# Kernel optimization log

Measured on AMD Instinct MI355X. Metric: run time of the kernel, lower is better.

The kernel has to match this reference:

```python
import jax, jax.numpy as jnp
import numpy as np

B, C, CO, N = 2, 32, 32, 64
MODES, LMAX, RBINS = 16, 2, 16
HALF = MODES // 2
NL = (LMAX + 1) ** 2  # 9 real spherical harmonics up to l=2
M = MODES ** 3
HID = 16  # round(CO * 0.5)


def _build_basis():
    # frequencies of the kept FNO corner modes along each axis
    f = np.concatenate([np.arange(HALF), np.arange(-HALF, 0)]).astype(np.float32)
    kx, ky, kz = np.meshgrid(f, f, f, indexing='ij')
    kx, ky, kz = kx.ravel(), ky.ravel(), kz.ravel()
    r = np.sqrt(kx ** 2 + ky ** 2 + kz ** 2)
    nzm = (r > 0).astype(np.float32)
    inv = np.where(r > 0, 1.0 / np.maximum(r, 1e-9), 0.0)
    ux, uy, uz = kx * inv, ky * inv, kz * inv
    # real spherical harmonics l=0,1,2 (cartesian form); all l>0 vanish at DC
    Y = np.stack([
        0.282095 * np.ones_like(r),
        0.488603 * uy, 0.488603 * uz, 0.488603 * ux,
        1.092548 * ux * uy, 1.092548 * uy * uz,
        0.315392 * (3.0 * uz ** 2 - nzm),
        1.092548 * ux * uz, 0.546274 * (ux ** 2 - uy ** 2)], axis=0)  # [NL, M]
    shell = np.minimum((r / (r.max() + 1e-6) * RBINS).astype(np.int64), RBINS - 1)
    cnt = np.bincount(shell, minlength=RBINS).astype(np.float32)
    w = 1.0 / np.sqrt(np.maximum(cnt, 1.0))
    mask = (shell[None, :] == np.arange(RBINS)[:, None]).astype(np.float32) * w[:, None]  # [RBINS, M]
    return (mask[:, None, :] * Y[None]).reshape(RBINS * NL, M).astype(np.float32)

BASIS = jnp.asarray(_build_basis())  # [K=144, M=4096], fixed projection basis
IDX = jnp.asarray(np.concatenate([np.arange(HALF), np.arange(N - HALF, N)]))  # kept mode indices


def cgelu(z):
    return jax.nn.gelu(z.real) + 1j * jax.nn.gelu(z.imag)


def setup_inputs() -> dict:
    key = jax.random.key(0)
    ks = jax.random.split(key, 17)
    rn = lambda k, s: jax.random.normal(k, s, dtype=jnp.float32)
    return {
        'x': rn(ks[0], (B, C, N, N, N)),
        'w_fno_r': rn(ks[1], (CO, C)) * 0.1, 'w_fno_i': rn(ks[2], (CO, C)) * 0.1,
        'b_fno_r': rn(ks[3], (CO,)) * 0.1, 'b_fno_i': rn(ks[4], (CO,)) * 0.1,
        'w_gate_r': rn(ks[5], (CO,)), 'w_gate_i': rn(ks[6], (CO,)),
        'w_spec_r': rn(ks[7], (RBINS, NL, C, CO)) * 0.1, 'w_spec_i': rn(ks[8], (RBINS, NL, C, CO)) * 0.1,
        'mlp_w1_r': rn(ks[9], (HID, CO)) * 0.1, 'mlp_w1_i': rn(ks[10], (HID, CO)) * 0.1,
        'mlp_b1_r': rn(ks[11], (HID,)) * 0.1, 'mlp_b1_i': rn(ks[12], (HID,)) * 0.1,
        'mlp_w2_r': rn(ks[13], (CO, HID)) * 0.1, 'mlp_w2_i': rn(ks[14], (CO, HID)) * 0.1,
        'mlp_b2_r': rn(ks[15], (CO,)) * 0.1, 'mlp_b2_i': rn(ks[16], (CO,)) * 0.1,
    }


def reference(x, w_fno_r, w_fno_i, b_fno_r, b_fno_i, w_gate_r, w_gate_i,
              w_spec_r, w_spec_i, mlp_w1_r, mlp_w1_i, mlp_b1_r, mlp_b1_i,
              mlp_w2_r, mlp_w2_i, mlp_b2_r, mlp_b2_i):
    cx = lambda r, i: (r + 1j * i).astype(jnp.complex64)
    xc = x.astype(jnp.complex64)
    w_fno, b_fno = cx(w_fno_r, w_fno_i), cx(b_fno_r, b_fno_i)
    w_gate = cx(w_gate_r, w_gate_i)
    w_spec = cx(w_spec_r, w_spec_i)
    w1, b1 = cx(mlp_w1_r, mlp_w1_i), cx(mlp_b1_r, mlp_b1_i)
    w2, b2 = cx(mlp_w2_r, mlp_w2_i), cx(mlp_b2_r, mlp_b2_i)

    # skip paths: complex 1x1-conv ('linear') and complex soft-gating
    skip_fno = jnp.einsum('oc,bcxyz->boxyz', w_fno, xc) + b_fno[None, :, None, None, None]
    skip_mlp = xc * w_gate[None, :, None, None, None]

    # Harmonic layer: FFT -> slice kept modes -> harmonic/radial projection
    # -> complex spectral conv -> inverse projection -> scatter -> iFFT
    xf = jnp.fft.fftn(xc, axes=(-3, -2, -1))
    xs = xf[:, :, IDX[:, None, None], IDX[None, :, None], IDX[None, None, :]].reshape(B, C, M)
    coeffs = jnp.einsum('bcm,km->bck', xs, BASIS).reshape(B, C, RBINS, NL)
    coeffs = jnp.einsum('bisl,slio->bosl', coeffs, w_spec)
    xs2 = jnp.einsum('bck,km->bcm', coeffs.reshape(B, CO, RBINS * NL), BASIS)
    full = jnp.zeros((B, CO, N, N, N), jnp.complex64).at[
        :, :, IDX[:, None, None], IDX[None, :, None], IDX[None, None, :]
    ].set(xs2.reshape(B, CO, MODES, MODES, MODES))
    x_fno = jnp.fft.ifftn(full, axes=(-3, -2, -1))

    x1 = x_fno + skip_fno  # n_layers=1 -> no activation here
    h = cgelu(jnp.einsum('hc,bcxyz->bhxyz', w1, x1) + b1[None, :, None, None, None])
    y = jnp.einsum('oh,bhxyz->boxyz', w2, h) + b2[None, :, None, None, None]
    return (y + skip_mlp).real
```

## Files before the change

### kernel.cpp

```cpp
#include <hip/hip_runtime.h>
#include <hip/hip_bf16.h>

#define PI2 6.283185307179586f

typedef __attribute__((ext_vector_type(8))) short short8;
typedef __attribute__((ext_vector_type(4))) float f32x4;

static const size_t O_Y      = 0;
static const size_t O_W1RT   = 36864;
static const size_t O_W1IT   = 37376;
static const size_t O_W1XR   = 37888;
static const size_t O_W1XI   = 38400;
static const size_t O_B1PR   = 38912;
static const size_t O_B1PI   = 38928;
static const size_t O_WSH    = 38944;
static const size_t O_SHELL  = 38960;
static const size_t O_ORDER  = 43056;
static const size_t O_SSTART = 47152;
static const size_t O_COEF   = 47232;
static const size_t O_COEF2  = 65664;
static const size_t O_XS     = 84096;
static const size_t O_XS2    = 608384;
static const size_t O_T2     = 1132672;
static const size_t O_T1     = 3229824;

static __device__ __forceinline__ float geluf(float v) {
  float u = 0.7978845608028654f * (v + 0.044715f * v * v * v);
  float a = fabsf(u);
  float e = __expf(-2.0f * a);
  float th = (1.0f - e) / (1.0f + e);
  th = copysignf(th, u);
  return 0.5f * v * (1.0f + th);
}

static __device__ __forceinline__ unsigned int f2bfbits(float f) {
  unsigned int u = __float_as_uint(f);
  u += 0x7fffu + ((u >> 16) & 1u);
  return u >> 16;
}

static __device__ __forceinline__ unsigned int pk2(float a, float b) {
  return f2bfbits(a) | (f2bfbits(b) << 16);
}

__global__ __launch_bounds__(256) void k0_init(
    const float* __restrict__ wfr, const float* __restrict__ wfi,
    const float* __restrict__ bfr, const float* __restrict__ bfi,
    const float* __restrict__ w1r, const float* __restrict__ w1i,
    const float* __restrict__ b1r, const float* __restrict__ b1i,
    float* __restrict__ ws) {
  float* Y    = ws + O_Y;
  float* w1rt = ws + O_W1RT;  float* w1it = ws + O_W1IT;
  float* W1xr = ws + O_W1XR;  float* W1xi = ws + O_W1XI;
  float* b1pr = ws + O_B1PR;  float* b1pi = ws + O_B1PI;
  float* wsh  = ws + O_WSH;
  int* shellOf = (int*)(ws + O_SHELL);
  int* order   = (int*)(ws + O_ORDER);
  int* sstart  = (int*)(ws + O_SSTART);

  __shared__ int cnt[16], fill[16], st[17];
  int tid = threadIdx.x;
  if (tid < 16) { cnt[tid] = 0; fill[tid] = 0; }
  __syncthreads();
  for (int m = tid; m < 4096; m += 256) {
    int ix = m >> 8, iy = (m >> 4) & 15, iz = m & 15;
    float kx = (float)(ix < 8 ? ix : ix - 16);
    float ky = (float)(iy < 8 ? iy : iy - 16);
    float kz = (float)(iz < 8 ? iz : iz - 16);
    float r2 = kx*kx + ky*ky + kz*kz;
    float r  = sqrtf(r2);
    float nzm = r2 > 0.f ? 1.f : 0.f;
    float inv = r2 > 0.f ? 1.0f / fmaxf(r, 1e-9f) : 0.f;
    float ux = kx*inv, uy = ky*inv, uz = kz*inv;
    Y[0*4096+m] = 0.282095f;
    Y[1*4096+m] = 0.488603f * uy;
    Y[2*4096+m] = 0.488603f * uz;
    Y[3*4096+m] = 0.488603f * ux;
    Y[4*4096+m] = 1.092548f * ux*uy;
    Y[5*4096+m] = 1.092548f * uy*uz;
    Y[6*4096+m] = 0.315392f * (3.0f*uz*uz - nzm);
    Y[7*4096+m] = 1.092548f * ux*uz;
    Y[8*4096+m] = 0.546274f * (ux*ux - uy*uy);
    float rmax = sqrtf(192.0f);
    float t = r / (rmax + 1e-6f) * 16.0f;
    int sh = (int)t; sh = sh > 15 ? 15 : sh;
    shellOf[m] = sh;
    atomicAdd(&cnt[sh], 1);
  }
  __syncthreads();
  if (tid == 0) { int a = 0; for (int s = 0; s < 16; ++s) { st[s] = a; a += cnt[s]; } st[16] = a; }
  __syncthreads();
  if (tid < 16) wsh[tid] = 1.0f / sqrtf(fmaxf((float)cnt[tid], 1.0f));
  if (tid < 17) sstart[tid] = st[tid];
  for (int m = tid; m < 4096; m += 256) {
    int sh = shellOf[m];
    int p = atomicAdd(&fill[sh], 1);
    order[st[sh] + p] = m;
  }
  for (int e = tid; e < 512; e += 256) {
    int j = e >> 5, c = e & 31;
    float ar = 0.f, ai = 0.f;
    for (int o = 0; o < 32; ++o) {
      float wr_ = w1r[j*32+o], wi_ = w1i[j*32+o];
      float fr  = wfr[o*32+c], fi_ = wfi[o*32+c];
      ar += wr_*fr - wi_*fi_;
      ai += wr_*fi_ + wi_*fr;
    }
    W1xr[c*16+j] = ar;  W1xi[c*16+j] = ai;
    w1rt[c*16+j] = w1r[j*32+c];
    w1it[c*16+j] = w1i[j*32+c];
  }
  if (tid < 16) {
    int j = tid;
    float ar = b1r[j], ai = b1i[j];
    for (int o = 0; o < 32; ++o) {
      ar += w1r[j*32+o]*bfr[o] - w1i[j*32+o]*bfi[o];
      ai += w1r[j*32+o]*bfi[o] + w1i[j*32+o]*bfr[o];
    }
    b1pr[j] = ar; b1pi[j] = ai;
  }
}

__global__ __launch_bounds__(256) void k12_fwd(const float* __restrict__ x, float* __restrict__ T2) {
  __shared__ __align__(16) float zS[4096];
  __shared__ float2 slab[64*17];
  __shared__ float2 tw[16*17];
  float* zP = zS;  float* zQ = zS + 1024;  float* zB = zS + 2048;  float* zD = zS + 3072;
  float* ysum = zS;
  int blk = blockIdx.x;
  const float* src = x + (size_t)blk * 4096;
  int tid = threadIdx.x;

  {
    int y = tid >> 2, zt = tid & 3;
    const float4* s4 = (const float4*)(src + y*64);
    float4 u0 = s4[zt];
    float4 u1 = s4[zt + 4];
    float4 u2 = s4[zt + 8];
    float4 u3 = s4[zt + 12];
    const float* p0 = (const float*)&u0; const float* p1 = (const float*)&u1;
    const float* p2 = (const float*)&u2; const float* p3 = (const float*)&u3;
    int base = 4*zt*64 + y;
    #pragma unroll
    for (int e = 0; e < 4; ++e) {
      float a = p0[e] + p2[e], c = p1[e] + p3[e];
      float bb = p0[e] - p2[e], d = p1[e] - p3[e];
      zP[base + e*64] = a + c;
      zQ[base + e*64] = a - c;
      zB[base + e*64] = bb;
      zD[base + e*64] = d;
    }
  }
  {
    int k = tid >> 4, i2 = tid & 15;
    float f = (float)(k < 8 ? k : k - 16);
    float ang = -PI2 * f * (float)i2 / 64.0f;
    float sw, cw; __sincosf(ang, &sw, &cw);
    tw[k*17 + i2] = make_float2(cw, sw);
  }
  __syncthreads();

  {
    int kz = tid & 15, yq = tid >> 4;
    int j = kz & 3;
    const float2* twp = tw + kz*17;
    float arr[4] = {0.f,0.f,0.f,0.f}, aii[4] = {0.f,0.f,0.f,0.f};
    if ((j & 1) == 0) {
      const float* plane = (j == 0) ? zP : zQ;
      #pragma unroll
      for (int z0 = 0; z0 < 16; ++z0) {
        float2 w = twp[z0];
        float4 s = *(const float4*)&plane[z0*64 + 4*yq];
        arr[0] += s.x*w.x; aii[0] += s.x*w.y;
        arr[1] += s.y*w.x; aii[1] += s.y*w.y;
        arr[2] += s.z*w.x; aii[2] += s.z*w.y;
        arr[3] += s.w*w.x; aii[3] += s.w*w.y;
      }
    } else {
      float dsg = (j == 1) ? -1.f : 1.f;
      #pragma unroll
      for (int z0 = 0; z0 < 16; ++z0) {
        float2 w = twp[z0];
        float4 b = *(const float4*)&zB[z0*64 + 4*yq];
        float4 d = *(const float4*)&zD[z0*64 + 4*yq];
        float swi = dsg * w.y, swr = dsg * w.x;
        arr[0] += b.x*w.x - d.x*swi;  aii[0] += b.x*w.y + d.x*swr;
        arr[1] += b.y*w.x - d.y*swi;  aii[1] += b.y*w.y + d.y*swr;
        arr[2] += b.z*w.x - d.z*swi;  aii[2] += b.z*w.y + d.z*swr;
        arr[3] += b.w*w.x - d.w*swi;  aii[3] += b.w*w.y + d.w*swr;
      }
    }
    int y0 = 4*yq;
    slab[(y0+0)*17 + kz] = make_float2(arr[0], aii[0]);
    slab[(y0+1)*17 + kz] = make_float2(arr[1], aii[1]);
    slab[(y0+2)*17 + kz] = make_float2(arr[2], aii[2]);
    slab[(y0+3)*17 + kz] = make_float2(arr[3], aii[3]);
  }
  __syncthreads();

  {
    int y0 = tid >> 4, kz = tid & 15;
    float2 u0 = slab[(y0     )*17 + kz];
    float2 u1 = slab[(y0 + 16)*17 + kz];
    float2 u2 = slab[(y0 + 32)*17 + kz];
    float2 u3 = slab[(y0 + 48)*17 + kz];
    float Ar = u0.x + u2.x, Ai = u0.y + u2.y;
    float Br = u0.x - u2.x, Bi = u0.y - u2.y;
    float Cr = u1.x + u3.x, Ci = u1.y + u3.y;
    float Dr = u1.x - u3.x, Di = u1.y - u3.y;
    float* yp = ysum + y0*162 + kz*10;
    yp[0] = Ar + Cr;  yp[1] = Ai + Ci;
    yp[2] = Br + Di;  yp[3] = Bi - Dr;
    yp[4] = Ar - Cr;  yp[5] = Ai - Ci;
    yp[6] = Br - Di;  yp[7] = Bi + Dr;
  }
  __syncthreads();

  {
    int kz = tid & 15, kyi = tid >> 4;
    const float* yp = ysum + kz*10 + (kyi & 3)*2;
    const float2* twp = tw + kyi*17;
    float ar = 0.f, ai = 0.f;
    #pragma unroll
    for (int y0 = 0; y0 < 16; ++y0) {
      float sr = yp[y0*162], si = yp[y0*162 + 1];
      float2 w = twp[y0];
      ar += sr*w.x - si*w.y;
      ai += sr*w.y + si*w.x;
    }
    *(float2*)&T2[(size_t)blk*512 + (kyi*16 + kz)*2] = make_float2(ar, ai);
  }
}

__global__ __launch_bounds__(256) void k3_dftx(const float* __restrict__ T2, float* __restrict__ xs) {
  __shared__ float slab[64*34];
  __shared__ float xsum[2592];
  __shared__ float2 twx[16*17];
  int blk = blockIdx.x;
  int bc = blk >> 4, ky = blk & 15;
  int tid = threadIdx.x;
  for (int i = tid; i < 2048; i += 256) {
    int xr = i >> 5, rem = i & 31;
    slab[xr*34 + rem] = T2[((size_t)(bc*64 + xr)*16 + ky)*32 + rem];
  }
  {
    int k = tid >> 4, i2 = tid & 15;
    float f = (float)(k < 8 ? k : k - 16);
    float ang = -PI2 * f * (float)i2 / 64.0f;
    float sw, cw; __sincosf(ang, &sw, &cw);
    twx[k*17 + i2] = make_float2(cw, sw);
  }
  __syncthreads();
  {
    int x0 = tid >> 4, kz = tid & 15;
    const float2* sp = (const float2*)slab;
    float2 u0 = sp[(x0     )*17 + kz];
    float2 u1 = sp[(x0 + 16)*17 + kz];
    float2 u2 = sp[(x0 + 32)*17 + kz];
    float2 u3 = sp[(x0 + 48)*17 + kz];
    float Ar = u0.x + u2.x, Ai = u0.y + u2.y;
    float Br = u0.x - u2.x, Bi = u0.y - u2.y;
    float Cr = u1.x + u3.x, Ci = u1.y + u3.y;
    float Dr = u1.x - u3.x, Di = u1.y - u3.y;
    float* yp = xsum + x0*162 + kz*10;
    yp[0] = Ar + Cr;  yp[1] = Ai + Ci;
    yp[2] = Br + Di;  yp[3] = Bi - Dr;
    yp[4] = Ar - Cr;  yp[5] = Ai - Ci;
    yp[6] = Br - Di;  yp[7] = Bi + Dr;
  }
  __syncthreads();
  {
    int kz = tid & 15, kxi = tid >> 4;
    const float* yp = xsum + kz*10 + (kxi & 3)*2;
    const float2* twp = twx + kxi*17;
    float ar = 0.f, ai = 0.f;
    #pragma unroll
    for (int x0 = 0; x0 < 16; ++x0) {
      float sr = yp[x0*162], si = yp[x0*162 + 1];
      float2 w = twp[x0];
      ar += sr*w.x - si*w.y;
      ai += sr*w.y + si*w.x;
    }
    *(float2*)&xs[(size_t)bc*8192 + (kxi*256 + ky*16 + kz)*2] = make_float2(ar, ai);
  }
}

__global__ __launch_bounds__(256) void k4_proj(const float* __restrict__ xs, const float* __restrict__ Y,
    const int* __restrict__ order, const int* __restrict__ sstart, const float* __restrict__ wsh,
    float* __restrict__ coeffs) {
  int blk = blockIdx.x; int bc = blk >> 4, s = blk & 15;
  int tid = threadIdx.x;
  int st = sstart[s], en = sstart[s+1];
  float ar[9], ai[9];
  #pragma unroll
  for (int l = 0; l < 9; ++l) { ar[l] = 0.f; ai[l] = 0.f; }
  for (int ii = st + tid; ii < en; ii += 256) {
    int m = order[ii];
    float2 v = *(const float2*)&xs[(size_t)bc*8192 + m*2];
    #pragma unroll
    for (int l = 0; l < 9; ++l) {
      float yv = Y[l*4096 + m];
      ar[l] += yv * v.x; ai[l] += yv * v.y;
    }
  }
  __shared__ float red[256*19];
  #pragma unroll
  for (int l = 0; l < 9; ++l) { red[tid*19 + l] = ar[l]; red[tid*19 + 9 + l] = ai[l]; }
  __syncthreads();
  for (int r = 128; r >= 1; r >>= 1) {
    if (tid < r) {
      #pragma unroll
      for (int q = 0; q < 18; ++q) red[tid*19 + q] += red[(tid + r)*19 + q];
    }
    __syncthreads();
  }
  if (tid == 0) {
    float w = wsh[s];
    for (int l = 0; l < 9; ++l) {
      coeffs[((size_t)bc*144 + s*9 + l)*2]     = w * red[l];
      coeffs[((size_t)bc*144 + s*9 + l)*2 + 1] = w * red[9 + l];
    }
  }
}

__global__ __launch_bounds__(64) void k5_spec(const float* __restrict__ coeffs,
    const float* __restrict__ wsr, const float* __restrict__ wsi, float* __restrict__ coeffs2) {
  int blk = blockIdx.x;
  int b = blk / 144, sl = blk % 144;
  int o = threadIdx.x;
  if (o >= 32) return;
  float ar = 0.f, ai = 0.f;
  for (int i = 0; i < 32; ++i) {
    float cr = coeffs[((size_t)(b*32 + i)*144 + sl)*2];
    float ci = coeffs[((size_t)(b*32 + i)*144 + sl)*2 + 1];
    float wr = wsr[(sl*32 + i)*32 + o];
    float wi = wsi[(sl*32 + i)*32 + o];
    ar += cr*wr - ci*wi;
    ai += cr*wi + ci*wr;
  }
  const float sc = 1.0f / 262144.0f;
  coeffs2[((size_t)(b*32 + o)*144 + sl)*2]     = ar * sc;
  coeffs2[((size_t)(b*32 + o)*144 + sl)*2 + 1] = ai * sc;
}

__global__ __launch_bounds__(256) void k7_unproj(const float* __restrict__ coeffs2, const float* __restrict__ Y,
    const int* __restrict__ shellOf, const float* __restrict__ wsh, float* __restrict__ xs2) {
  int bo = blockIdx.x >> 4;
  int m = ((blockIdx.x & 15) << 8) | threadIdx.x;
  __shared__ float c2[288];
  for (int i = threadIdx.x; i < 288; i += 256) c2[i] = coeffs2[(size_t)bo*288 + i];
  __syncthreads();
  int sh = shellOf[m];
  float w = wsh[sh];
  float ar = 0.f, ai = 0.f;
  #pragma unroll
  for (int l = 0; l < 9; ++l) {
    float yv = Y[l*4096 + m];
    ar += yv * c2[(sh*9 + l)*2];
    ai += yv * c2[(sh*9 + l)*2 + 1];
  }
  xs2[(size_t)bo*8192 + m*2]     = w * ar;
  xs2[(size_t)bo*8192 + m*2 + 1] = w * ai;
}

__global__ __launch_bounds__(256) void k8_invx(const float* __restrict__ xs2, float* __restrict__ U1) {
  __shared__ float slab[512];
  int blk = blockIdx.x;
  int bo = blk >> 4, ky = blk & 15;
  int tid = threadIdx.x;
  for (int i = tid; i < 512; i += 256) {
    int kx = i >> 5, rem = i & 31;
    slab[i] = xs2[(size_t)bo*8192 + kx*512 + ky*32 + rem];
  }
  __syncthreads();
  int kz = tid & 15, grp = tid >> 4;
  float ang = PI2 * (float)grp / 64.0f;
  float sw, cw; __sincosf(ang, &sw, &cw);
  float tr = 1.f, ti = 0.f;
  float sjr[4] = {0.f,0.f,0.f,0.f}, sji[4] = {0.f,0.f,0.f,0.f};
  #pragma unroll
  for (int kx = 0; kx < 16; ++kx) {
    if (kx == 8) ti = -ti;
    float2 v = *(const float2*)&slab[(kx*16 + kz)*2];
    sjr[kx & 3] += v.x*tr - v.y*ti;
    sji[kx & 3] += v.x*ti + v.y*tr;
    float nt = tr*cw - ti*sw; ti = tr*sw + ti*cw; tr = nt;
  }
  float Ar = sjr[0]+sjr[2], Ai = sji[0]+sji[2];
  float Br = sjr[0]-sjr[2], Bi = sji[0]-sji[2];
  float Cr = sjr[1]+sjr[3], Ci = sji[1]+sji[3];
  float Dr = sjr[1]-sjr[3], Di = sji[1]-sji[3];
  *(float2*)&U1[((size_t)(bo*64 + grp     )*16 + ky)*32 + kz*2] = make_float2(Ar+Cr, Ai+Ci);
  *(float2*)&U1[((size_t)(bo*64 + grp + 16)*16 + ky)*32 + kz*2] = make_float2(Br-Di, Bi+Dr);
  *(float2*)&U1[((size_t)(bo*64 + grp + 32)*16 + ky)*32 + kz*2] = make_float2(Ar-Cr, Ai-Ci);
  *(float2*)&U1[((size_t)(bo*64 + grp + 48)*16 + ky)*32 + kz*2] = make_float2(Br+Di, Bi-Dr);
}

__global__ __launch_bounds__(256) void k9_invy(const float* __restrict__ U1, float* __restrict__ U2) {
  __shared__ float slab[512];
  int blk = blockIdx.x;
  int tid = threadIdx.x;
  const float* src = U1 + (size_t)blk * 512;
  for (int i = tid; i < 512; i += 256) slab[i] = src[i];
  __syncthreads();
  int kz = tid & 15, grp = tid >> 4;
  float ang = PI2 * (float)grp / 64.0f;
  float sw, cw; __sincosf(ang, &sw, &cw);
  float tr = 1.f, ti = 0.f;
  float sjr[4] = {0.f,0.f,0.f,0.f}, sji[4] = {0.f,0.f,0.f,0.f};
  #pragma unroll
  for (int ky = 0; ky < 16; ++ky) {
    if (ky == 8) ti = -ti;
    float2 v = *(const float2*)&slab[(ky*16 + kz)*2];
    sjr[ky & 3] += v.x*tr - v.y*ti;
    sji[ky & 3] += v.x*ti + v.y*tr;
    float nt = tr*cw - ti*sw; ti = tr*sw + ti*cw; tr = nt;
  }
  float Ar = sjr[0]+sjr[2], Ai = sji[0]+sji[2];
  float Br = sjr[0]-sjr[2], Bi = sji[0]-sji[2];
  float Cr = sjr[1]+sjr[3], Ci = sji[1]+sji[3];
  float Dr = sjr[1]-sjr[3], Di = sji[1]-sji[3];
  float* dst = U2 + (size_t)blk * 2048;
  *(float2*)&dst[((grp     )*16 + kz)*2] = make_float2(Ar+Cr, Ai+Ci);
  *(float2*)&dst[((grp + 16)*16 + kz)*2] = make_float2(Br-Di, Bi+Dr);
  *(float2*)&dst[((grp + 32)*16 + kz)*2] = make_float2(Ar-Cr, Ai-Ci);
  *(float2*)&dst[((grp + 48)*16 + kz)*2] = make_float2(Br+Di, Bi-Dr);
}

__global__ __launch_bounds__(256) void k10_final(
    const float* __restrict__ x, const float* __restrict__ U2,
    const float* __restrict__ ws,
    const float* __restrict__ w2r, const float* __restrict__ w2i,
    const float* __restrict__ b2r, const float* __restrict__ wgr,
    float* __restrict__ out) {
  const float* w1rt = ws + O_W1RT;  const float* w1it = ws + O_W1IT;
  const float* W1xr = ws + O_W1XR;  const float* W1xi = ws + O_W1XI;
  const float* b1pr = ws + O_B1PR;  const float* b1pi = ws + O_B1PI;

  __shared__ unsigned int xfT[128*33];
  __shared__ __hip_bfloat16 xlT[128*34];
  __shared__ f32x4 hpW4[272];
  unsigned int* hpW = (unsigned int*)hpW4;
  float* scratch = (float*)xfT;

  int tid = threadIdx.x;
  int blk = blockIdx.x;
  int yb = blk & 31, bx = blk >> 5;
  int b = bx >> 6, xr = bx & 63;
  int y0 = yb * 2;

  for (int i = tid; i < 1024; i += 256) {
    int ya = i >> 9, c = (i >> 4) & 31, zq = i & 15;
    const float4 v = *(const float4*)&x[(size_t)(b*32 + c)*262144 + (size_t)xr*4096
                                        + (size_t)(y0 + ya)*64 + 4*zq];
    int rb = ((ya << 6) + 4*zq)*34 + c;
    xlT[rb]       = __float2bfloat16(v.x);
    xlT[rb + 34]  = __float2bfloat16(v.y);
    xlT[rb + 68]  = __float2bfloat16(v.z);
    xlT[rb + 102] = __float2bfloat16(v.w);
  }
  for (int e = tid; e < 1024; e += 256) {
    int q = e & 15, o = (e >> 4) & 31, ya = e >> 9;
    const float2* g = (const float2*)(U2 + ((size_t)((b*32 + o)*64 + xr))*2048 + (size_t)(y0 + ya)*32);
    *(float2*)&scratch[(ya*32 + o)*34 + 2*q] = g[q];
  }
  if (tid < 128) {
    int k2 = tid >> 4, i2 = tid & 15;
    int ka = 2*k2, kb = ka + 1;
    float f0 = (float)(ka < 8 ? ka : ka - 16);
    float f1 = (float)(kb < 8 ? kb : kb - 16);
    float s0, c0, s1, c1;
    __sincosf(PI2 * f0 * (float)i2 / 64.0f, &s0, &c0);
    __sincosf(PI2 * f1 * (float)i2 / 64.0f, &s1, &c1);
    hpW4[k2*17 + i2] = (f32x4){c0, s0, c1, s1};
  }
  __syncthreads();

  {
    int o = tid & 31, r3 = tid >> 5;
    int ya = r3 >> 2, zq = r3 & 3;
    float ur[16], ui[16];
    const float2* sp = (const float2*)&scratch[(ya*32 + o)*34];
    #pragma unroll
    for (int q = 0; q < 16; ++q) { float2 v = sp[q]; ur[q] = v.x; ui[q] = v.y; }
    __syncthreads();

    const f32x4* twz4 = (const f32x4*)hpW4;
    #pragma unroll
    for (int t = 0; t < 4; ++t) {
      int z0 = 4*zq + t;
      float sr[4] = {0.f, 0.f, 0.f, 0.f}, si[4] = {0.f, 0.f, 0.f, 0.f};
      #pragma unroll
      for (int k2 = 0; k2 < 8; ++k2) {
        f32x4 w = twz4[k2*17 + z0];
        int ka = 2*k2, kb = ka + 1;
        sr[ka & 3] += ur[ka]*w[0] - ui[ka]*w[1];
        si[ka & 3] += ur[ka]*w[1] + ui[ka]*w[0];
        sr[kb & 3] += ur[kb]*w[2] - ui[kb]*w[3];
        si[kb & 3] += ur[kb]*w[3] + ui[kb]*w[2];
      }
      float Ar = sr[0]+sr[2], Ai = si[0]+si[2];
      float Br = sr[0]-sr[2], Bi = si[0]-si[2];
      float Cr = sr[1]+sr[3], Ci = si[1]+si[3];
      float Dr = sr[1]-sr[3], Di = si[1]-si[3];
      int rb = (ya << 6) + z0;
      xfT[rb*33 + o]        = pk2(Ar+Cr, Ai+Ci);
      xfT[(rb+16)*33 + o]   = pk2(Br-Di, Bi+Dr);
      xfT[(rb+32)*33 + o]   = pk2(Ar-Cr, Ai-Ci);
      xfT[(rb+48)*33 + o]   = pk2(Br+Di, Bi-Dr);
    }
  }
  __syncthreads();

  {
    int lane = tid & 63, wv = tid >> 6;
    int p = lane & 15, q = lane >> 4;
    int wb = wv * 272;

    union U8 { short8 v; unsigned int u[4]; };
    U8 fW1r, fW1i, fW1iN, fW1xr, fW1xi, fW2[2];
    #pragma unroll
    for (int s = 0; s < 4; ++s) {
      int c0 = 8*q + 2*s, c1 = c0 + 1;
      fW1r.u[s]  = pk2(w1rt[c0*16 + p], w1rt[c1*16 + p]);
      fW1i.u[s]  = pk2(w1it[c0*16 + p], w1it[c1*16 + p]);
      fW1iN.u[s] = fW1i.u[s] ^ 0x80008000u;
      fW1xr.u[s] = pk2(W1xr[c0*16 + p], W1xr[c1*16 + p]);
      fW1xi.u[s] = pk2(W1xi[c0*16 + p], W1xi[c1*16 + p]);
    }
    #pragma unroll
    for (int mt = 0; mt < 2; ++mt) {
      int o = mt*16 + p;
      #pragma unroll
      for (int s = 0; s < 4; ++s) {
        int k0 = 8*q + 2*s;
        float a  = (k0   < 16) ? w2r[o*16 + k0]      : -w2i[o*16 + k0 - 16];
        float bb = (k0+1 < 16) ? w2r[o*16 + k0 + 1]  : -w2i[o*16 + k0 - 15];
        fW2[mt].u[s] = pk2(a, bb);
      }
    }
    float4 b1r4 = *(const float4*)(b1pr + 4*q);
    float4 b1i4 = *(const float4*)(b1pi + 4*q);
    float b2a[2][4], wga[2][4];
    #pragma unroll
    for (int mt = 0; mt < 2; ++mt) {
      float4 t0 = *(const float4*)(b2r + mt*16 + 4*q);
      float4 t1 = *(const float4*)(wgr + mt*16 + 4*q);
      b2a[mt][0]=t0.x; b2a[mt][1]=t0.y; b2a[mt][2]=t0.z; b2a[mt][3]=t0.w;
      wga[mt][0]=t1.x; wga[mt][1]=t1.y; wga[mt][2]=t1.z; wga[mt][3]=t1.w;
    }
    float b1ra[4] = {b1r4.x, b1r4.y, b1r4.z, b1r4.w};
    float b1ia[4] = {b1i4.x, b1i4.y, b1i4.z, b1i4.w};

    f32x4 zacc = {0.f, 0.f, 0.f, 0.f};
    const unsigned int* xlW = (const unsigned int*)xlT;

    for (int tt = 0; tt < 2; ++tt) {
      int tile = wv*2 + tt;
      int ya = tile >> 2, zg = tile & 3;
      int row = ya*64 + zg*16 + p;

      unsigned int w8[8];
      #pragma unroll
      for (int jj = 0; jj < 8; ++jj) w8[jj] = xfT[row*33 + 8*q + jj];
      U8 FR, FI, XV;
      #pragma unroll
      for (int s = 0; s < 4; ++s) {
        FR.u[s] = __builtin_amdgcn_perm(w8[2*s+1], w8[2*s], 0x05040100u);
        FI.u[s] = __builtin_amdgcn_perm(w8[2*s+1], w8[2*s], 0x07060302u);
        XV.u[s] = xlW[row*17 + 4*q + s];
      }

      f32x4 accR = zacc, accI = zacc;
      accR = __builtin_amdgcn_mfma_f32_16x16x32_bf16(fW1r.v,  FR.v, accR, 0, 0, 0);
      accR = __builtin_amdgcn_mfma_f32_16x16x32_bf16(fW1iN.v, FI.v, accR, 0, 0, 0);
      accR = __builtin_amdgcn_mfma_f32_16x16x32_bf16(fW1xr.v, XV.v, accR, 0, 0, 0);
      accI = __builtin_amdgcn_mfma_f32_16x16x32_bf16(fW1r.v,  FI.v, accI, 0, 0, 0);
      accI = __builtin_amdgcn_mfma_f32_16x16x32_bf16(fW1i.v,  FR.v, accI, 0, 0, 0);
      accI = __builtin_amdgcn_mfma_f32_16x16x32_bf16(fW1xi.v, XV.v, accI, 0, 0, 0);

      float hr_[4], hi_[4];
      #pragma unroll
      for (int r = 0; r < 4; ++r) {
        hr_[r] = geluf(accR[r] + b1ra[r]);
        hi_[r] = geluf(accI[r] + b1ia[r]);
      }
      hpW[wb + 17*p + 2*q]     = pk2(hr_[0], hr_[1]);
      hpW[wb + 17*p + 2*q + 1] = pk2(hr_[2], hr_[3]);
      hpW[wb + 17*p + 8 + 2*q]     = pk2(hi_[0], hi_[1]);
      hpW[wb + 17*p + 8 + 2*q + 1] = pk2(hi_[2], hi_[3]);

      U8 FH;
      #pragma unroll
      for (int s = 0; s < 4; ++s) FH.u[s] = hpW[wb + 17*p + 4*q + s];

      #pragma unroll
      for (int mt = 0; mt < 2; ++mt) {
        f32x4 accO = __builtin_amdgcn_mfma_f32_16x16x32_bf16(fW2[mt].v, FH.v, zacc, 0, 0, 0);
        #pragma unroll
        for (int r = 0; r < 4; ++r) {
          int o = mt*16 + q*4 + r;
          int z = zg*16 + p;
          float xv = __bfloat162float(xlT[row*34 + o]);
          out[(size_t)(b*32 + o)*262144 + (size_t)xr*4096 + (size_t)(y0 + ya)*64 + z]
              = accO[r] + b2a[mt][r] + wga[mt][r]*xv;
        }
      }
    }
  }
}

extern "C" void kernel_launch(void* const* d_in, const int* in_sizes, int n_in,
                              void* d_out, int out_size, void* d_ws, size_t ws_size,
                              hipStream_t stream) {
  (void)in_sizes; (void)n_in; (void)out_size; (void)ws_size;
  const float* x   = (const float*)d_in[0];
  const float* wfr = (const float*)d_in[1];
  const float* wfi = (const float*)d_in[2];
  const float* bfr = (const float*)d_in[3];
  const float* bfi = (const float*)d_in[4];
  const float* wgr = (const float*)d_in[5];
  const float* wsr = (const float*)d_in[7];
  const float* wsi = (const float*)d_in[8];
  const float* w1r = (const float*)d_in[9];
  const float* w1i = (const float*)d_in[10];
  const float* b1r = (const float*)d_in[11];
  const float* b1i = (const float*)d_in[12];
  const float* w2r = (const float*)d_in[13];
  const float* w2i = (const float*)d_in[14];
  const float* b2r = (const float*)d_in[15];
  float* out = (float*)d_out;
  float* ws  = (float*)d_ws;

  float* T1      = ws + O_T1;
  float* T2      = ws + O_T2;
  float* xs      = ws + O_XS;
  float* xs2     = ws + O_XS2;
  float* coeffs  = ws + O_COEF;
  float* coeffs2 = ws + O_COEF2;
  float* Y       = ws + O_Y;
  int* shellOf   = (int*)(ws + O_SHELL);
  int* order     = (int*)(ws + O_ORDER);
  int* sstart    = (int*)(ws + O_SSTART);
  float* wsh     = ws + O_WSH;

  hipLaunchKernelGGL(k0_init,  dim3(1),    dim3(256), 0, stream, wfr, wfi, bfr, bfi, w1r, w1i, b1r, b1i, ws);
  hipLaunchKernelGGL(k12_fwd,  dim3(4096), dim3(256), 0, stream, x, T2);
  hipLaunchKernelGGL(k3_dftx,  dim3(1024), dim3(256), 0, stream, T2, xs);
  hipLaunchKernelGGL(k4_proj,  dim3(1024), dim3(256), 0, stream, xs, Y, order, sstart, wsh, coeffs);
  hipLaunchKernelGGL(k5_spec,  dim3(288),  dim3(64),  0, stream, coeffs, wsr, wsi, coeffs2);
  hipLaunchKernelGGL(k7_unproj,dim3(1024), dim3(256), 0, stream, coeffs2, Y, shellOf, wsh, xs2);
  hipLaunchKernelGGL(k8_invx,  dim3(1024), dim3(256), 0, stream, xs2, T2);
  hipLaunchKernelGGL(k9_invy,  dim3(4096), dim3(256), 0, stream, T2, T1);
  hipLaunchKernelGGL(k10_final,dim3(4096), dim3(256), 0, stream, x, T1, ws, w2r, w2i, b2r, wgr, out);
}
```

Measured before the change: 269.2 us.

## Fuse spectral conv, unprojection and inverse DFTs into fewer kernels

Merges the spectral channel mix, the inverse harmonic projection and the inverse x-DFT into one kernel, and folds the inverse y-DFT into the final MLP kernel, removing the xs2, coeffs2 and T1 intermediates and two launches. The projection reduction moves from a shared-memory tree to wavefront shuffles. A small pre-transpose of the spectral weights is added so reads are coalesced. The cost is that each block recomputes the 32-channel spectral mix for its (b,o), and the final kernel now does the y-DFT from a staged U1 with extra syncs.

```diff
diff --git a/kernel.cpp b/kernel.cpp
--- a/kernel.cpp
+++ b/kernel.cpp
@@ -18,11 +18,9 @@
 static const size_t O_ORDER  = 43056;
 static const size_t O_SSTART = 47152;
 static const size_t O_COEF   = 47232;
-static const size_t O_COEF2  = 65664;
 static const size_t O_XS     = 84096;
-static const size_t O_XS2    = 608384;
+static const size_t O_WST    = 608384;
 static const size_t O_T2     = 1132672;
-static const size_t O_T1     = 3229824;
 
 static __device__ __forceinline__ float geluf(float v) {
   float u = 0.7978845608028654f * (v + 0.044715f * v * v * v);
@@ -121,6 +119,17 @@
   }
 }
 
+__global__ __launch_bounds__(256) void k0b_wst(const float* __restrict__ wsr,
+    const float* __restrict__ wsi, float* __restrict__ ws) {
+  float* wst = ws + O_WST;
+  int o = blockIdx.x;
+  for (int e = threadIdx.x; e < 4608; e += 256) {
+    int i = e / 144, sl = e - i*144;
+    wst[(size_t)o*9216 + i*288 + sl*2]     = wsr[(sl*32 + i)*32 + o];
+    wst[(size_t)o*9216 + i*288 + sl*2 + 1] = wsi[(sl*32 + i)*32 + o];
+  }
+}
+
 __global__ __launch_bounds__(256) void k12_fwd(const float* __restrict__ x, float* __restrict__ T2) {
   __shared__ __align__(16) float zS[4096];
   __shared__ float2 slab[64*17];
@@ -303,76 +312,78 @@
       ar[l] += yv * v.x; ai[l] += yv * v.y;
     }
   }
-  __shared__ float red[256*19];
-  #pragma unroll
-  for (int l = 0; l < 9; ++l) { red[tid*19 + l] = ar[l]; red[tid*19 + 9 + l] = ai[l]; }
-  __syncthreads();
-  for (int r = 128; r >= 1; r >>= 1) {
-    if (tid < r) {
-      #pragma unroll
-      for (int q = 0; q < 18; ++q) red[tid*19 + q] += red[(tid + r)*19 + q];
-    }
-    __syncthreads();
-  }
-  if (tid == 0) {
-    float w = wsh[s];
-    for (int l = 0; l < 9; ++l) {
-      coeffs[((size_t)bc*144 + s*9 + l)*2]     = w * red[l];
-      coeffs[((size_t)bc*144 + s*9 + l)*2 + 1] = w * red[9 + l];
-    }
-  }
-}
-
-__global__ __launch_bounds__(64) void k5_spec(const float* __restrict__ coeffs,
-    const float* __restrict__ wsr, const float* __restrict__ wsi, float* __restrict__ coeffs2) {
-  int blk = blockIdx.x;
-  int b = blk / 144, sl = blk % 144;
-  int o = threadIdx.x;
-  if (o >= 32) return;
-  float ar = 0.f, ai = 0.f;
-  for (int i = 0; i < 32; ++i) {
-    float cr = coeffs[((size_t)(b*32 + i)*144 + sl)*2];
-    float ci = coeffs[((size_t)(b*32 + i)*144 + sl)*2 + 1];
-    float wr = wsr[(sl*32 + i)*32 + o];
-    float wi = wsi[(sl*32 + i)*32 + o];
-    ar += cr*wr - ci*wi;
-    ai += cr*wi + ci*wr;
-  }
-  const float sc = 1.0f / 262144.0f;
-  coeffs2[((size_t)(b*32 + o)*144 + sl)*2]     = ar * sc;
-  coeffs2[((size_t)(b*32 + o)*144 + sl)*2 + 1] = ai * sc;
-}
-
-__global__ __launch_bounds__(256) void k7_unproj(const float* __restrict__ coeffs2, const float* __restrict__ Y,
-    const int* __restrict__ shellOf, const float* __restrict__ wsh, float* __restrict__ xs2) {
-  int bo = blockIdx.x >> 4;
-  int m = ((blockIdx.x & 15) << 8) | threadIdx.x;
-  __shared__ float c2[288];
-  for (int i = threadIdx.x; i < 288; i += 256) c2[i] = coeffs2[(size_t)bo*288 + i];
-  __syncthreads();
-  int sh = shellOf[m];
-  float w = wsh[sh];
-  float ar = 0.f, ai = 0.f;
   #pragma unroll
   for (int l = 0; l < 9; ++l) {
-    float yv = Y[l*4096 + m];
-    ar += yv * c2[(sh*9 + l)*2];
-    ai += yv * c2[(sh*9 + l)*2 + 1];
-  }
-  xs2[(size_t)bo*8192 + m*2]     = w * ar;
-  xs2[(size_t)bo*8192 + m*2 + 1] = w * ai;
-}
-
-__global__ __launch_bounds__(256) void k8_invx(const float* __restrict__ xs2, float* __restrict__ U1) {
+    #pragma unroll
+    for (int d = 1; d < 64; d <<= 1) {
+      ar[l] += __shfl_xor(ar[l], d, 64);
+      ai[l] += __shfl_xor(ai[l], d, 64);
+    }
+  }
+  __shared__ float wred[4][18];
+  int wv = tid >> 6, lane = tid & 63;
+  if (lane == 0) {
+    #pragma unroll
+    for (int l = 0; l < 9; ++l) { wred[wv][l] = ar[l]; wred[wv][9 + l] = ai[l]; }
+  }
+  __syncthreads();
+  if (tid < 18) {
+    float sum = wred[0][tid] + wred[1][tid] + wred[2][tid] + wred[3][tid];
+    float w = wsh[s];
+    int l = tid < 9 ? tid : tid - 9;
+    int ri = tid < 9 ? 0 : 1;
+    coeffs[((size_t)bc*144 + s*9 + l)*2 + ri] = w * sum;
+  }
+}
+
+__global__ __launch_bounds__(256) void k857(const float* __restrict__ coeffs,
+    const float* __restrict__ ws, float* __restrict__ U1) {
+  const float* wst = ws + O_WST;
+  const float* Y   = ws + O_Y;
+  const int* shellOf = (const int*)(ws + O_SHELL);
+  const float* wsh = ws + O_WSH;
+  __shared__ float c2[288];
   __shared__ float slab[512];
   int blk = blockIdx.x;
   int bo = blk >> 4, ky = blk & 15;
+  int b = bo >> 5, o = bo & 31;
   int tid = threadIdx.x;
-  for (int i = tid; i < 512; i += 256) {
-    int kx = i >> 5, rem = i & 31;
-    slab[i] = xs2[(size_t)bo*8192 + kx*512 + ky*32 + rem];
-  }
-  __syncthreads();
+
+  if (tid < 144) {
+    int sl = tid;
+    const float* cp = coeffs + ((size_t)b*4608 + sl)*2;
+    const float* wp = wst + (size_t)o*9216 + sl*2;
+    float ar = 0.f, ai = 0.f;
+    #pragma unroll 4
+    for (int i = 0; i < 32; ++i) {
+      float cr = cp[i*288], ci = cp[i*288 + 1];
+      float wr = wp[i*288], wi = wp[i*288 + 1];
+      ar += cr*wr - ci*wi;
+      ai += cr*wi + ci*wr;
+    }
+    const float sc = 1.0f / 262144.0f;
+    c2[sl*2]     = ar * sc;
+    c2[sl*2 + 1] = ai * sc;
+  }
+  __syncthreads();
+
+  {
+    int kxi = tid >> 4, kz = tid & 15;
+    int m = kxi*256 + ky*16 + kz;
+    int sh = shellOf[m];
+    float w = wsh[sh];
+    float ar = 0.f, ai = 0.f;
+    #pragma unroll
+    for (int l = 0; l < 9; ++l) {
+      float yv = Y[l*4096 + m];
+      ar += yv * c2[(sh*9 + l)*2];
+      ai += yv * c2[(sh*9 + l)*2 + 1];
+    }
+    slab[tid*2]     = w * ar;
+    slab[tid*2 + 1] = w * ai;
+  }
+  __syncthreads();
+
   int kz = tid & 15, grp = tid >> 4;
   float ang = PI2 * (float)grp / 64.0f;
   float sw, cw; __sincosf(ang, &sw, &cw);
@@ -396,39 +407,8 @@
   *(float2*)&U1[((size_t)(bo*64 + grp + 48)*16 + ky)*32 + kz*2] = make_float2(Br+Di, Bi-Dr);
 }
 
-__global__ __launch_bounds__(256) void k9_invy(const float* __restrict__ U1, float* __restrict__ U2) {
-  __shared__ float slab[512];
-  int blk = blockIdx.x;
-  int tid = threadIdx.x;
-  const float* src = U1 + (size_t)blk * 512;
-  for (int i = tid; i < 512; i += 256) slab[i] = src[i];
-  __syncthreads();
-  int kz = tid & 15, grp = tid >> 4;
-  float ang = PI2 * (float)grp / 64.0f;
-  float sw, cw; __sincosf(ang, &sw, &cw);
-  float tr = 1.f, ti = 0.f;
-  float sjr[4] = {0.f,0.f,0.f,0.f}, sji[4] = {0.f,0.f,0.f,0.f};
-  #pragma unroll
-  for (int ky = 0; ky < 16; ++ky) {
-    if (ky == 8) ti = -ti;
-    float2 v = *(const float2*)&slab[(ky*16 + kz)*2];
-    sjr[ky & 3] += v.x*tr - v.y*ti;
-    sji[ky & 3] += v.x*ti + v.y*tr;
-    float nt = tr*cw - ti*sw; ti = tr*sw + ti*cw; tr = nt;
-  }
-  float Ar = sjr[0]+sjr[2], Ai = sji[0]+sji[2];
-  float Br = sjr[0]-sjr[2], Bi = sji[0]-sji[2];
-  float Cr = sjr[1]+sjr[3], Ci = sji[1]+sji[3];
-  float Dr = sjr[1]-sjr[3], Di = sji[1]-sji[3];
-  float* dst = U2 + (size_t)blk * 2048;
-  *(float2*)&dst[((grp     )*16 + kz)*2] = make_float2(Ar+Cr, Ai+Ci);
-  *(float2*)&dst[((grp + 16)*16 + kz)*2] = make_float2(Br-Di, Bi+Dr);
-  *(float2*)&dst[((grp + 32)*16 + kz)*2] = make_float2(Ar-Cr, Ai-Ci);
-  *(float2*)&dst[((grp + 48)*16 + kz)*2] = make_float2(Br+Di, Bi-Dr);
-}
-
 __global__ __launch_bounds__(256) void k10_final(
-    const float* __restrict__ x, const float* __restrict__ U2,
+    const float* __restrict__ x, const float* __restrict__ U1,
     const float* __restrict__ ws,
     const float* __restrict__ w2r, const float* __restrict__ w2i,
     const float* __restrict__ b2r, const float* __restrict__ wgr,
@@ -437,11 +417,13 @@
   const float* W1xr = ws + O_W1XR;  const float* W1xi = ws + O_W1XI;
   const float* b1pr = ws + O_B1PR;  const float* b1pi = ws + O_B1PI;
 
-  __shared__ unsigned int xfT[128*33];
+  __shared__ __align__(16) unsigned int xfT[128*33];
   __shared__ __hip_bfloat16 xlT[128*34];
+  __shared__ float2 scr2[2*32*17];
   __shared__ f32x4 hpW4[272];
   unsigned int* hpW = (unsigned int*)hpW4;
-  float* scratch = (float*)xfT;
+  float2* u1h = (float2*)xfT;
+  float2* twY = (float2*)(hpW4 + 160);
 
   int tid = threadIdx.x;
   int blk = blockIdx.x;
@@ -459,11 +441,6 @@
     xlT[rb + 68]  = __float2bfloat16(v.z);
     xlT[rb + 102] = __float2bfloat16(v.w);
   }
-  for (int e = tid; e < 1024; e += 256) {
-    int q = e & 15, o = (e >> 4) & 31, ya = e >> 9;
-    const float2* g = (const float2*)(U2 + ((size_t)((b*32 + o)*64 + xr))*2048 + (size_t)(y0 + ya)*32);
-    *(float2*)&scratch[(ya*32 + o)*34 + 2*q] = g[q];
-  }
   if (tid < 128) {
     int k2 = tid >> 4, i2 = tid & 15;
     int ka = 2*k2, kb = ka + 1;
@@ -473,6 +450,36 @@
     __sincosf(PI2 * f0 * (float)i2 / 64.0f, &s0, &c0);
     __sincosf(PI2 * f1 * (float)i2 / 64.0f, &s1, &c1);
     hpW4[k2*17 + i2] = (f32x4){c0, s0, c1, s1};
+  } else if (tid < 160) {
+    int t = tid - 128;
+    int ky = t >> 1, ya = t & 1;
+    float f = (float)(ky < 8 ? ky : ky - 16);
+    float sw, cw; __sincosf(PI2 * f * (float)(y0 + ya) / 64.0f, &sw, &cw);
+    twY[t] = make_float2(cw, sw);
+  }
+
+  for (int oq = 0; oq < 4; ++oq) {
+    __syncthreads();
+    for (int i = tid; i < 1024; i += 256) {
+      int ol = i >> 7, r = i & 127;
+      ((float4*)u1h)[ol*128 + r] =
+          *(const float4*)&U1[((size_t)((b*32 + oq*8 + ol)*64 + xr))*512 + 4*r];
+    }
+    __syncthreads();
+    if (tid < 128) {
+      int kz = tid & 15, ol = tid >> 4;
+      float2 a0 = make_float2(0.f, 0.f), a1 = make_float2(0.f, 0.f);
+      #pragma unroll
+      for (int ky = 0; ky < 16; ++ky) {
+        float2 u = u1h[(ol*16 + ky)*16 + kz];
+        float2 w0 = twY[ky*2], w1 = twY[ky*2 + 1];
+        a0.x += u.x*w0.x - u.y*w0.y;  a0.y += u.x*w0.y + u.y*w0.x;
+        a1.x += u.x*w1.x - u.y*w1.y;  a1.y += u.x*w1.y + u.y*w1.x;
+      }
+      int o = oq*8 + ol;
+      scr2[(o     )*17 + kz] = a0;
+      scr2[(32 + o)*17 + kz] = a1;
+    }
   }
   __syncthreads();
 
@@ -480,10 +487,9 @@
     int o = tid & 31, r3 = tid >> 5;
     int ya = r3 >> 2, zq = r3 & 3;
     float ur[16], ui[16];
-    const float2* sp = (const float2*)&scratch[(ya*32 + o)*34];
+    const float2* sp = &scr2[(ya*32 + o)*17];
     #pragma unroll
     for (int q = 0; q < 16; ++q) { float2 v = sp[q]; ur[q] = v.x; ui[q] = v.y; }
-    __syncthreads();
 
     const f32x4* twz4 = (const f32x4*)hpW4;
     #pragma unroll
@@ -632,25 +638,19 @@
   float* out = (float*)d_out;
   float* ws  = (float*)d_ws;
 
-  float* T1      = ws + O_T1;
   float* T2      = ws + O_T2;
   float* xs      = ws + O_XS;
-  float* xs2     = ws + O_XS2;
   float* coeffs  = ws + O_COEF;
-  float* coeffs2 = ws + O_COEF2;
   float* Y       = ws + O_Y;
-  int* shellOf   = (int*)(ws + O_SHELL);
   int* order     = (int*)(ws + O_ORDER);
   int* sstart    = (int*)(ws + O_SSTART);
   float* wsh     = ws + O_WSH;
 
   hipLaunchKernelGGL(k0_init,  dim3(1),    dim3(256), 0, stream, wfr, wfi, bfr, bfi, w1r, w1i, b1r, b1i, ws);
+  hipLaunchKernelGGL(k0b_wst,  dim3(32),   dim3(256), 0, stream, wsr, wsi, ws);
   hipLaunchKernelGGL(k12_fwd,  dim3(4096), dim3(256), 0, stream, x, T2);
   hipLaunchKernelGGL(k3_dftx,  dim3(1024), dim3(256), 0, stream, T2, xs);
   hipLaunchKernelGGL(k4_proj,  dim3(1024), dim3(256), 0, stream, xs, Y, order, sstart, wsh, coeffs);
-  hipLaunchKernelGGL(k5_spec,  dim3(288),  dim3(64),  0, stream, coeffs, wsr, wsi, coeffs2);
-  hipLaunchKernelGGL(k7_unproj,dim3(1024), dim3(256), 0, stream, coeffs2, Y, shellOf, wsh, xs2);
-  hipLaunchKernelGGL(k8_invx,  dim3(1024), dim3(256), 0, stream, xs2, T2);
-  hipLaunchKernelGGL(k9_invy,  dim3(4096), dim3(256), 0, stream, T2, T1);
-  hipLaunchKernelGGL(k10_final,dim3(4096), dim3(256), 0, stream, x, T1, ws, w2r, w2i, b2r, wgr, out);
-}
+  hipLaunchKernelGGL(k857,     dim3(1024), dim3(256), 0, stream, coeffs, ws, T2);
+  hipLaunchKernelGGL(k10_final,dim3(4096), dim3(256), 0, stream, x, T2, ws, w2r, w2i, b2r, wgr, out);
+}
```

Result: slower. 287.9 us (+7.0%).
